# Kernel tuning notes

Hardware: AMD Instinct MI355X
Metric: run time of the kernel (lower is better)

The kernel has to match this reference:

```python
import jax, jax.numpy as jnp
import numpy as np

DIM = 1024
HEADS = 16
DIM_HEAD = 64
DIM_INNER = HEADS * DIM_HEAD
R_MAJOR = 2.0
R_MINOR = 1.0
EPS = 1e-10
ATTN_SCALE = DIM_HEAD ** 0.5  # torch SDPA `scale` is a multiplier on q@k^T
S_QK_FACTOR = float(DIM)      # Scale forward multiplier: init / scale = 1.0 / (1/dim)


def toroidal_norm(t, axis=-1, R=R_MAJOR, r=R_MINOR, eps=EPS):
    """Project onto sphere, scale first half of `axis` by R, second by r, renormalize."""
    axis = axis % t.ndim
    n = jnp.linalg.norm(t, axis=axis, keepdims=True)
    sp = t / jnp.clip(n, eps)
    d = t.shape[axis]
    h = d // 2
    scale = jnp.concatenate([jnp.full((h,), R, t.dtype), jnp.full((d - h,), r, t.dtype)])
    bshape = [1] * t.ndim
    bshape[axis] = d
    tp = sp * scale.reshape(bshape)
    n2 = jnp.linalg.norm(tp, axis=axis, keepdims=True)
    return tp / jnp.clip(n2, eps)


def setup_inputs() -> dict:
    key = jax.random.key(0)
    ks = jax.random.split(key, 5)
    b, n = 4, 1024
    x = jax.random.normal(ks[0], (b, n, DIM), jnp.float32)
    std = DIM ** -0.5
    w_q = jax.random.normal(ks[1], (DIM_INNER, DIM), jnp.float32) * std
    w_k = jax.random.normal(ks[2], (DIM_INNER, DIM), jnp.float32) * std
    w_v = jax.random.normal(ks[3], (DIM_INNER, DIM), jnp.float32) * std
    w_o = jax.random.normal(ks[4], (DIM, DIM_INNER), jnp.float32) * std
    qk_scale_param = jnp.full((DIM_INNER,), 1.0 / DIM, jnp.float32)  # Scale init
    return {"x": x, "w_q": w_q, "w_k": w_k, "w_v": w_v, "w_o": w_o,
            "qk_scale_param": qk_scale_param}


def reference(x, w_q, w_k, w_v, w_o, qk_scale_param):
    b, n, _ = x.shape
    # parametrized (toroidal-normed) projection weights
    wq = toroidal_norm(w_q, axis=-1)
    wk = toroidal_norm(w_k, axis=-1)
    wv = toroidal_norm(w_v, axis=-1)
    wo = toroidal_norm(w_o, axis=0)  # norm_dim_in=False -> dim=0

    q = jnp.einsum('bnd,ed->bne', x, wq).reshape(b, n, HEADS, DIM_HEAD).transpose(0, 2, 1, 3)
    k = jnp.einsum('bnd,ed->bne', x, wk).reshape(b, n, HEADS, DIM_HEAD).transpose(0, 2, 1, 3)
    v = jnp.einsum('bnd,ed->bne', x, wv).reshape(b, n, HEADS, DIM_HEAD).transpose(0, 2, 1, 3)

    # toroidal norm over head dim
    q = toroidal_norm(q, axis=-1)
    k = toroidal_norm(k, axis=-1)

    # learned per-channel qk scale: param * (init / scale)
    s = (qk_scale_param * S_QK_FACTOR).reshape(HEADS, 1, DIM_HEAD)
    q = q * s

    scores = jnp.einsum('bhnd,bhmd->bhnm', q, k) * ATTN_SCALE
    causal = jnp.tril(jnp.ones((n, n), bool))
    scores = jnp.where(causal, scores, jnp.finfo(scores.dtype).min)
    attn = jax.nn.softmax(scores, axis=-1)
    out = jnp.einsum('bhnm,bhmd->bhnd', attn, v)  # b h n d

    out = out.transpose(0, 2, 1, 3).reshape(b, n, DIM_INNER)
    return jnp.einsum('bne,de->bnd', out, wo)
```

## Files before the change

kernel.cpp:

```cpp
#include <hip/hip_runtime.h>
#include <hip/hip_bf16.h>

#define HEADS 16
#define DH    64
#define BATCH 4
#define SEQ   1024
#define DIMD  1024
#define TOK   4096

typedef __attribute__((ext_vector_type(8))) short bf16x8;
typedef __attribute__((ext_vector_type(4))) float f32x4;
typedef __attribute__((ext_vector_type(16))) float f32x16;

typedef const void __attribute__((address_space(1)))* gas1_t;
typedef void __attribute__((address_space(3)))* las3_t;

#define GLOAD16(g,l) __builtin_amdgcn_global_load_lds((gas1_t)(g),(las3_t)(l),16,0,0)
#define MFMA_BF16(a,b,c) __builtin_amdgcn_mfma_f32_16x16x32_bf16((a),(b),(c),0,0,0)
#define MFMA32(a,b,c) __builtin_amdgcn_mfma_f32_32x32x16_bf16((a),(b),(c),0,0,0)
#define ZERO16 {0.f,0.f,0.f,0.f,0.f,0.f,0.f,0.f,0.f,0.f,0.f,0.f,0.f,0.f,0.f,0.f}

__device__ __forceinline__ ushort f2bf(float f){
  __hip_bfloat16 h = __float2bfloat16(f);
  return *reinterpret_cast<ushort*>(&h);
}
__device__ __forceinline__ uint packbf2(float a, float b){
  return (uint)f2bf(a) | ((uint)f2bf(b) << 16);
}
__device__ __forceinline__ uint xswap32(uint x){
  return (uint)__shfl_xor((int)x, 32);
}

__global__ __launch_bounds__(256) void prep_kernel(
    const float* __restrict__ x,
    const float* __restrict__ wq, const float* __restrict__ wk, const float* __restrict__ wv,
    const float* __restrict__ wo,
    ushort* __restrict__ xb,
    ushort* __restrict__ oq, ushort* __restrict__ ok, ushort* __restrict__ ov,
    ushort* __restrict__ wob, float* __restrict__ part)
{
  __shared__ float sp[4];
  int bid = blockIdx.x, t = threadIdx.x;
  if (bid < 2048){
    int i = bid*256 + t;
    const float4* x4 = (const float4*)x;
    float4 a = x4[2*i], b = x4[2*i+1];
    union { ushort s[8]; uint4 u; } uu;
    uu.s[0]=f2bf(a.x); uu.s[1]=f2bf(a.y); uu.s[2]=f2bf(a.z); uu.s[3]=f2bf(a.w);
    uu.s[4]=f2bf(b.x); uu.s[5]=f2bf(b.y); uu.s[6]=f2bf(b.z); uu.s[7]=f2bf(b.w);
    ((uint4*)xb)[i] = uu.u;
  } else if (bid < 5120){
    int bb = bid - 2048;
    int row = bb & 1023;
    int m = bb >> 10;
    const float* src = (m==0)?wq:((m==1)?wk:wv);
    ushort* dst = (m==0)?oq:((m==1)?ok:ov);
    float4 v = ((const float4*)(src + (size_t)row*1024))[t];
    float sc = (t<128)?2.f:1.f;
    float ss = sc*sc*(v.x*v.x + v.y*v.y + v.z*v.z + v.w*v.w);
    #pragma unroll
    for (int off=1; off<64; off<<=1) ss += __shfl_xor(ss, off);
    int w = t>>6, lane = t&63;
    if (lane==0) sp[w]=ss;
    __syncthreads();
    float tot = sp[0]+sp[1]+sp[2]+sp[3];
    float inv = rsqrtf(fmaxf(tot,1e-20f)) * sc;
    union { ushort s[4]; uint2 u; } o;
    o.s[0]=f2bf(v.x*inv); o.s[1]=f2bf(v.y*inv); o.s[2]=f2bf(v.z*inv); o.s[3]=f2bf(v.w*inv);
    ((uint2*)(dst + (size_t)row*1024))[t] = o.u;
  } else if (bid < 5632){
    int i = (bid-5120)*256 + t;
    float sc = ((i>>7) < 512) ? 2.f : 1.f;
    const float4* x4 = (const float4*)wo;
    float4 a = x4[2*i], b = x4[2*i+1];
    union { ushort s[8]; uint4 u; } uu;
    uu.s[0]=f2bf(a.x*sc); uu.s[1]=f2bf(a.y*sc); uu.s[2]=f2bf(a.z*sc); uu.s[3]=f2bf(a.w*sc);
    uu.s[4]=f2bf(b.x*sc); uu.s[5]=f2bf(b.y*sc); uu.s[6]=f2bf(b.z*sc); uu.s[7]=f2bf(b.w*sc);
    ((uint4*)wob)[i] = uu.u;
  } else {
    int rb = bid - 5632;
    float4 a = {0.f,0.f,0.f,0.f};
    #pragma unroll 4
    for (int r=0;r<32;r++){
      int row = rb*32+r;
      float4 v = ((const float4*)wo)[row*256 + t];
      float s2 = (row<512)?4.f:1.f;
      a.x += s2*v.x*v.x; a.y += s2*v.y*v.y; a.z += s2*v.z*v.z; a.w += s2*v.w*v.w;
    }
    ((float4*)part)[rb*256 + t] = a;
  }
}

__global__ __launch_bounds__(256) void wo_csum_kernel(const float* __restrict__ part,
                                                      float* __restrict__ colsum){
  int c = blockIdx.x*256 + threadIdx.x;
  float s = 0.f;
  #pragma unroll
  for (int j=0;j<32;j++) s += part[j*1024 + c];
  colsum[c] = s;
}

template<int NZ>
__global__ __launch_bounds__(256, 2) void gemm_fused_kernel(
    const ushort* __restrict__ A,
    const ushort* __restrict__ B0, const ushort* __restrict__ B1, const ushort* __restrict__ B2,
    void* dst0, void* dst1, void* dst2,
    const float* __restrict__ qparam, const float* __restrict__ colsum, int K)
{
  __shared__ ushort As[64*32];
  __shared__ ushort Bs[NZ*128*32];
  const int bm = blockIdx.x*64, bn = blockIdx.y*128;
  const int tid = threadIdx.x, lane = tid&63, w = tid>>6;
  const int wr = w>>1, wc = w&1;
  const int l15 = lane&15, l4 = lane>>4;
  const int srow = lane>>2, sch = lane&3;
  const int scol = (sch ^ (srow&3))*8;

  const f32x4 zero4 = {0.f,0.f,0.f,0.f};
  f32x4 acc[NZ][2][4];
  #pragma unroll
  for (int z=0;z<NZ;z++)
    #pragma unroll
    for (int m=0;m<2;m++)
      #pragma unroll
      for (int n=0;n<4;n++) acc[z][m][n] = zero4;

  for (int k0=0; k0<K; k0+=32){
    __syncthreads();
    GLOAD16(A + (size_t)(bm + w*16 + srow)*K + k0 + scol, &As[w*512]);
    #pragma unroll
    for (int j=0;j<NZ*2;j++){
      int seg = j*4 + w;
      int z = seg>>3, s = seg&7;
      const ushort* Bp = (z==0)?B0:((z==1)?B1:B2);
      GLOAD16(Bp + (size_t)(bn + s*16 + srow)*K + k0 + scol, &Bs[seg*512]);
    }
    __syncthreads();
    bf16x8 af[2];
    #pragma unroll
    for (int m=0;m<2;m++)
      af[m] = *(const bf16x8*)&As[(wr*32 + m*16 + l15)*32 + ((l4 ^ (l15&3))*8)];
    #pragma unroll
    for (int z=0;z<NZ;z++){
      bf16x8 bfr[4];
      #pragma unroll
      for (int n=0;n<4;n++)
        bfr[n] = *(const bf16x8*)&Bs[z*4096 + (wc*64 + n*16 + l15)*32 + ((l4 ^ (l15&3))*8)];
      #pragma unroll
      for (int m=0;m<2;m++)
        #pragma unroll
        for (int n=0;n<4;n++)
          acc[z][m][n] = MFMA_BF16(af[m], bfr[n], acc[z][m][n]);
    }
  }

  if (NZ==3){
    #pragma unroll
    for (int z=0;z<3;z++){
      ushort* dst = (ushort*)((z==0)?dst0:((z==1)?dst1:dst2));
      float qs[4];
      #pragma unroll
      for (int n=0;n<4;n++){
        int e = bn + wc*64 + n*16 + l15;
        if (z==0)      qs[n] = qparam[e]*8192.f*1.44269504088896f;
        else if (z==2) qs[n] = rsqrtf(fmaxf(colsum[e],1e-20f));
        else           qs[n] = 1.f;
      }
      #pragma unroll
      for (int m=0;m<2;m++){
        float ssq[4] = {0.f,0.f,0.f,0.f};
        if (z<2){
          #pragma unroll
          for (int reg=0;reg<4;reg++){
            float s=0.f;
            #pragma unroll
            for (int n=0;n<4;n++){
              float scl2 = (n<2)?4.f:1.f;
              float vv = acc[z][m][n][reg];
              s += scl2*vv*vv;
            }
            ssq[reg]=s;
          }
          #pragma unroll
          for (int d=1; d<16; d<<=1){
            #pragma unroll
            for (int reg=0;reg<4;reg++) ssq[reg] += __shfl_xor(ssq[reg], d);
          }
        }
        #pragma unroll
        for (int n=0;n<4;n++){
          float scl = (n<2)?2.f:1.f;
          #pragma unroll
          for (int reg=0;reg<4;reg++){
            float val = acc[z][m][n][reg];
            if (z<2) val = val*scl*rsqrtf(fmaxf(ssq[reg],1e-20f))*qs[n];
            else     val = val*qs[n];
            int row = bm + wr*32 + m*16 + l4*4 + reg;
            int col = bn + wc*64 + n*16 + l15;
            int b = row>>10, nn = row&1023, h = col>>6, d = col&63;
            if (z==2)
              dst[(((size_t)b*HEADS+h)*DH + d)*SEQ + nn] = f2bf(val);
            else
              dst[(((size_t)b*HEADS+h)*SEQ + nn)*DH + d] = f2bf(val);
          }
        }
      }
    }
  } else {
    float* outp = (float*)dst0;
    #pragma unroll
    for (int m=0;m<2;m++)
      #pragma unroll
      for (int n=0;n<4;n++)
        #pragma unroll
        for (int reg=0;reg<4;reg++){
          int row = bm + wr*32 + m*16 + l4*4 + reg;
          int col = bn + wc*64 + n*16 + l15;
          outp[(size_t)row*DIMD + col] = acc[0][m][n][reg];
        }
  }
}

template<int NS, bool MASK>
__device__ __forceinline__ void attn_iter(
    const ushort* __restrict__ Kp, const ushort* __restrict__ Vp,
    int kvb, const bf16x8 (&qf)[4], int l31, int l1,
    f32x16& o0, f32x16& o1, float& m_s, float& l_s)
{
  bf16x8 kfa[4], kfb[4];
  #pragma unroll
  for (int md=0; md<4; md++)
    kfa[md] = *(const bf16x8*)&Kp[(size_t)(kvb + l31)*DH + md*16 + l1*8];
  if (NS==2){
    #pragma unroll
    for (int md=0; md<4; md++)
      kfb[md] = *(const bf16x8*)&Kp[(size_t)(kvb + 32 + l31)*DH + md*16 + l1*8];
  }
  bf16x8 vf0[2*NS], vf1[2*NS];
  #pragma unroll
  for (int kc=0; kc<2*NS; kc++){
    vf0[kc] = *(const bf16x8*)&Vp[(size_t)l31*SEQ      + kvb + kc*16 + l1*8];
    vf1[kc] = *(const bf16x8*)&Vp[(size_t)(32+l31)*SEQ + kvb + kc*16 + l1*8];
  }

  f32x16 s0 = ZERO16, s1 = ZERO16;
  __builtin_amdgcn_s_setprio(1);
  #pragma unroll
  for (int md=0; md<4; md++) s0 = MFMA32(kfa[md], qf[md], s0);
  if (NS==2){
    #pragma unroll
    for (int md=0; md<4; md++) s1 = MFMA32(kfb[md], qf[md], s1);
  }
  __builtin_amdgcn_s_setprio(0);

  if (MASK){
    f32x16& sm = (NS==2) ? s1 : s0;
    #pragma unroll
    for (int r=0;r<16;r++){
      int kvl = (r&3) + 8*(r>>2) + 4*l1;
      if (kvl > l31) sm[r] = -3.0e38f;
    }
  }

  float mx = -3.0e38f;
  #pragma unroll
  for (int r=0;r<16;r++) mx = fmaxf(mx, s0[r]);
  if (NS==2){
    #pragma unroll
    for (int r=0;r<16;r++) mx = fmaxf(mx, s1[r]);
  }
  mx = fmaxf(mx, __shfl_xor(mx, 32));
  float mnew = fmaxf(m_s, mx);
  float alpha = __builtin_amdgcn_exp2f(m_s - mnew);
  m_s = mnew;
  float rs = 0.f;
  #pragma unroll
  for (int r=0;r<16;r++){ s0[r] = __builtin_amdgcn_exp2f(s0[r]-mnew); rs += s0[r]; }
  if (NS==2){
    #pragma unroll
    for (int r=0;r<16;r++){ s1[r] = __builtin_amdgcn_exp2f(s1[r]-mnew); rs += s1[r]; }
  }
  rs += __shfl_xor(rs, 32);
  l_s = l_s*alpha + rs;

  #pragma unroll
  for (int r=0;r<16;r++){ o0[r] *= alpha; o1[r] *= alpha; }

  uint ru[16];
  #pragma unroll
  for (int j=0;j<8;j++) ru[j] = packbf2(s0[2*j], s0[2*j+1]);
  if (NS==2){
    #pragma unroll
    for (int j=0;j<8;j++) ru[8+j] = packbf2(s1[2*j], s1[2*j+1]);
  }
  union U4 { uint u[4]; bf16x8 v; };
  U4 fr[2*NS];
  #pragma unroll
  for (int j=0;j<NS;j++){
    uint px[8];
    #pragma unroll
    for (int k=0;k<8;k++) px[k] = xswap32(ru[8*j+k]);
    fr[2*j].u[0]   = l1 ? px[2]      : ru[8*j+0];
    fr[2*j].u[1]   = l1 ? px[3]      : ru[8*j+1];
    fr[2*j].u[2]   = l1 ? ru[8*j+2]  : px[0];
    fr[2*j].u[3]   = l1 ? ru[8*j+3]  : px[1];
    fr[2*j+1].u[0] = l1 ? px[6]      : ru[8*j+4];
    fr[2*j+1].u[1] = l1 ? px[7]      : ru[8*j+5];
    fr[2*j+1].u[2] = l1 ? ru[8*j+6]  : px[4];
    fr[2*j+1].u[3] = l1 ? ru[8*j+7]  : px[5];
  }

  __builtin_amdgcn_s_setprio(1);
  #pragma unroll
  for (int kc=0; kc<2*NS; kc++){
    o0 = MFMA32(vf0[kc], fr[kc].v, o0);
    o1 = MFMA32(vf1[kc], fr[kc].v, o1);
  }
  __builtin_amdgcn_s_setprio(0);
}

__device__ __forceinline__ void process_tile(
    int t, int par, int bh,
    const ushort* __restrict__ Q, const ushort* __restrict__ K,
    const ushort* __restrict__ VT, ushort* __restrict__ O,
    int l31, int l1)
{
  const size_t base  = (size_t)bh * SEQ * DH;
  const size_t vbase = (size_t)bh * DH * SEQ;
  const ushort* Kp = K + base;
  const ushort* Vp = VT + vbase;
  const int qbase = t*64 + par*32;

  bf16x8 qf[4];
  #pragma unroll
  for (int md=0; md<4; md++)
    qf[md] = *(const bf16x8*)&Q[base + (size_t)(qbase + l31)*DH + md*16 + l1*8];

  f32x16 o0 = ZERO16, o1 = ZERO16;
  float m_s = -3.0e38f, l_s = 0.f;

  for (int kt=0; kt<t; kt++)
    attn_iter<2,false>(Kp, Vp, kt*64, qf, l31, l1, o0, o1, m_s, l_s);
  if (par) attn_iter<2,true>(Kp, Vp, t*64, qf, l31, l1, o0, o1, m_s, l_s);
  else     attn_iter<1,true>(Kp, Vp, t*64, qf, l31, l1, o0, o1, m_s, l_s);

  float li = 1.0f / l_s;
  int b = bh >> 4, hh = bh & 15;
  int n = qbase + l31;
  ushort* orow = O + ((size_t)b*SEQ + n)*DIMD + hh*64;
  #pragma unroll
  for (int r=0;r<16;r++){
    int dl = (r&3) + 8*(r>>2) + 4*l1;
    orow[dl]    = f2bf(o0[r]*li);
    orow[32+dl] = f2bf(o1[r]*li);
  }
}

__global__ __launch_bounds__(256, 2) void attn_kernel(
    const ushort* __restrict__ Q, const ushort* __restrict__ K, const ushort* __restrict__ VT,
    ushort* __restrict__ O)
{
  int id = blockIdx.x;
  int p  = id >> 6;
  int r  = id & 63;
  int bh = (r&7)*8 + (r>>3);
  int tid = threadIdx.x, wi = tid>>6, lane = tid&63;
  int l31 = lane & 31, l1 = lane >> 5;
  int sel = (wi & 1) ^ (bh & 1);
  int t   = sel ? (15-p) : p;
  int par = wi >> 1;
  process_tile(t, par, bh, Q, K, VT, O, l31, l1);
}

extern "C" void kernel_launch(void* const* d_in, const int* in_sizes, int n_in,
                              void* d_out, int out_size, void* d_ws, size_t ws_size,
                              hipStream_t stream)
{
  const float* x      = (const float*)d_in[0];
  const float* w_q    = (const float*)d_in[1];
  const float* w_k    = (const float*)d_in[2];
  const float* w_v    = (const float*)d_in[3];
  const float* w_o    = (const float*)d_in[4];
  const float* qparam = (const float*)d_in[5];
  char* ws = (char*)d_ws;
  const size_t MB = 1u<<20;
  ushort* xb  = (ushort*)(ws);
  ushort* wqb = (ushort*)(ws + 8*MB);
  ushort* wkb = (ushort*)(ws + 10*MB);
  ushort* wvb = (ushort*)(ws + 12*MB);
  ushort* wob = (ushort*)(ws + 14*MB);
  ushort* qd  = (ushort*)(ws + 16*MB);
  ushort* kd  = (ushort*)(ws + 24*MB);
  ushort* vd  = (ushort*)(ws + 32*MB);
  ushort* att = xb;
  float* part = (float*)(ws + 40*MB);
  float* colsum = (float*)d_out + (out_size - 1024);

  prep_kernel<<<dim3(5664), dim3(256), 0, stream>>>(
      x, w_q, w_k, w_v, w_o, xb, wqb, wkb, wvb, wob, part);
  wo_csum_kernel<<<dim3(4), dim3(256), 0, stream>>>(part, colsum);
  gemm_fused_kernel<3><<<dim3(64,8), dim3(256), 0, stream>>>(
      xb, wqb, wkb, wvb, (void*)qd, (void*)kd, (void*)vd, qparam, colsum, DIMD);
  attn_kernel<<<dim3(512), dim3(256), 0, stream>>>(qd, kd, vd, att);
  gemm_fused_kernel<1><<<dim3(64,8), dim3(256), 0, stream>>>(
      att, wob, wob, wob, d_out, nullptr, nullptr, nullptr, nullptr, DIMD);
}
```

Before: 120.0 us.

## Double-buffer LDS tiles in fused GEMM to overlap global loads with MFMA

The fused projection GEMM now keeps two LDS buffers for the A and B tiles. It issues async global-to-LDS loads for the next K-slice before computing on the current one, and uses vmcnt waits and raw barriers in place of the two __syncthreads per iteration. This is meant to hide global memory latency behind matrix math. In exchange it doubles LDS use, which can lower occupancy under launch_bounds(256,2), and its correctness depends on the hand-counted vmcnt values.

```diff
diff --git a/kernel.cpp b/kernel.cpp
--- a/kernel.cpp
+++ b/kernel.cpp
@@ -107,8 +107,8 @@
     void* dst0, void* dst1, void* dst2,
     const float* __restrict__ qparam, const float* __restrict__ colsum, int K)
 {
-  __shared__ ushort As[64*32];
-  __shared__ ushort Bs[NZ*128*32];
+  __shared__ ushort As[2][2048];
+  __shared__ ushort Bs[2][NZ*4096];
   const int bm = blockIdx.x*64, bn = blockIdx.y*128;
   const int tid = threadIdx.x, lane = tid&63, w = tid>>6;
   const int wr = w>>1, wc = w&1;
@@ -125,34 +125,51 @@
       #pragma unroll
       for (int n=0;n<4;n++) acc[z][m][n] = zero4;
 
-  for (int k0=0; k0<K; k0+=32){
-    __syncthreads();
-    GLOAD16(A + (size_t)(bm + w*16 + srow)*K + k0 + scol, &As[w*512]);
+  auto stage = [&](int c, int k0){
+    GLOAD16(A + (size_t)(bm + w*16 + srow)*K + k0 + scol, &As[c][w*512]);
     #pragma unroll
     for (int j=0;j<NZ*2;j++){
       int seg = j*4 + w;
       int z = seg>>3, s = seg&7;
       const ushort* Bp = (z==0)?B0:((z==1)?B1:B2);
-      GLOAD16(Bp + (size_t)(bn + s*16 + srow)*K + k0 + scol, &Bs[seg*512]);
+      GLOAD16(Bp + (size_t)(bn + s*16 + srow)*K + k0 + scol, &Bs[c][seg*512]);
     }
-    __syncthreads();
+  };
+  auto compute = [&](int c){
     bf16x8 af[2];
     #pragma unroll
     for (int m=0;m<2;m++)
-      af[m] = *(const bf16x8*)&As[(wr*32 + m*16 + l15)*32 + ((l4 ^ (l15&3))*8)];
+      af[m] = *(const bf16x8*)&As[c][(wr*32 + m*16 + l15)*32 + ((l4 ^ (l15&3))*8)];
     #pragma unroll
     for (int z=0;z<NZ;z++){
       bf16x8 bfr[4];
       #pragma unroll
       for (int n=0;n<4;n++)
-        bfr[n] = *(const bf16x8*)&Bs[z*4096 + (wc*64 + n*16 + l15)*32 + ((l4 ^ (l15&3))*8)];
+        bfr[n] = *(const bf16x8*)&Bs[c][z*4096 + (wc*64 + n*16 + l15)*32 + ((l4 ^ (l15&3))*8)];
       #pragma unroll
       for (int m=0;m<2;m++)
         #pragma unroll
         for (int n=0;n<4;n++)
           acc[z][m][n] = MFMA_BF16(af[m], bfr[n], acc[z][m][n]);
     }
-  }
+  };
+
+  stage(0, 0);
+  asm volatile("s_waitcnt vmcnt(0)" ::: "memory");
+  __builtin_amdgcn_s_barrier();
+  int cur = 0;
+  for (int k0=32; k0<K; k0+=32){
+    stage(cur^1, k0);
+    if (NZ==3) asm volatile("s_waitcnt vmcnt(7)" ::: "memory");
+    else       asm volatile("s_waitcnt vmcnt(3)" ::: "memory");
+    __builtin_amdgcn_s_barrier();
+    compute(cur);
+    __builtin_amdgcn_s_barrier();
+    cur ^= 1;
+  }
+  asm volatile("s_waitcnt vmcnt(0)" ::: "memory");
+  __builtin_amdgcn_s_barrier();
+  compute(cur);
 
   if (NZ==3){
     #pragma unroll
```

Result: slower. 237.8 us (+98.2%).
